# Performance work log

Measured on AMD Instinct MI355X. Metric: run time of the kernel, lower is better.

Reference implementation:

```python
import jax, jax.numpy as jnp
import numpy as np

NUM_EMBEDDINGS = 512
EMBEDDING_DIM = 64
COMMITMENT_COST = 0.25


def setup_inputs() -> dict:
    key = jax.random.key(0)
    k1, k2 = jax.random.split(key)
    inputs = jax.random.normal(k1, (32, 64, 64, 64), dtype=jnp.float32)  # NCHW, C=D
    # torch init: uniform(-1/K, 1/K)
    embeddings = jax.random.uniform(
        k2, (NUM_EMBEDDINGS, EMBEDDING_DIM), dtype=jnp.float32,
        minval=-1.0 / NUM_EMBEDDINGS, maxval=1.0 / NUM_EMBEDDINGS)
    return {"inputs": inputs, "embeddings": embeddings}


def reference(inputs, embeddings):
    # NCHW -> NHWC
    x = jnp.transpose(inputs, (0, 2, 3, 1))
    B, H, W, D = x.shape
    flat = x.reshape(-1, D)  # [N, D]
    # squared L2 distances to codebook: [N, K]
    distances = (jnp.sum(flat * flat, axis=1, keepdims=True)
                 + jnp.sum(embeddings * embeddings, axis=1)
                 - 2.0 * flat @ embeddings.T)
    encoding_indices = jnp.argmin(distances, axis=1)  # [N]
    # one-hot @ codebook in the original == direct gather
    quantized = embeddings[encoding_indices].reshape(B, H, W, D)
    # commitment loss (quantized is detached in original)
    e_latent_loss = jnp.mean((jax.lax.stop_gradient(quantized) - x) ** 2)
    loss = COMMITMENT_COST * e_latent_loss
    # straight-through estimator
    quantized_st = x + jax.lax.stop_gradient(quantized - x)
    out = jnp.transpose(quantized_st, (0, 3, 1, 2))  # back to NCHW
    return out, loss, encoding_indices.reshape(B, H, W)
```

## Files before the change

### kernel.cpp

```cpp
#include <hip/hip_runtime.h>
#include <math.h>

#define NUM_K 512
#define DIM   64
#define HW    4096
#define IMG   (DIM * HW)
#define OUT_Q 8388608
#define LOSS_OFF OUT_Q
#define IDX_OFF (OUT_Q + 1)
#define DELTA 8e-5f

#define WS_EH   0
#define WS_EL   65536
#define WS_SE   131072
#define WS_CNT  133120
#define WS_PART 133376
#define WS_ET   137472
#define WS_WL   268544

typedef float f32x4 __attribute__((ext_vector_type(4)));
typedef short s8v   __attribute__((ext_vector_type(8)));

__device__ inline short f2bf(float f) {
  unsigned u = __float_as_uint(f);
  return (short)((u + 0x7FFF + ((u >> 16) & 1)) >> 16);
}
__device__ inline float bf2f(short s) {
  return __uint_as_float(((unsigned)(unsigned short)s) << 16);
}

__global__ void vq_prep(const float* __restrict__ emb, char* __restrict__ ws) {
  short* eh = (short*)(ws + WS_EH);
  short* el = (short*)(ws + WS_EL);
  float* se = (float*)(ws + WS_SE);
  float* et = (float*)(ws + WS_ET);
  __shared__ float ebuf[64][65];
  const int tid = threadIdx.x;
  const int kb  = blockIdx.x * 64;
  if (blockIdx.x == 0 && tid == 0) *(int*)(ws + WS_CNT) = 0;
#pragma unroll
  for (int i = 0; i < 64; ++i)
    ebuf[i][tid] = emb[(size_t)(kb + i) * DIM + tid];
  __syncthreads();
  const int k = kb + tid;
  float s = 0.f;
#pragma unroll
  for (int j = 0; j < DIM; ++j) {
    const float v = ebuf[tid][j];
    s = fmaf(v, v, s);
    const short h = f2bf(v);
    eh[k * DIM + j] = h;
    el[k * DIM + j] = f2bf(v - bf2f(h));
    et[j * NUM_K + k] = v;
  }
  se[k] = s;
}

__launch_bounds__(512, 4)
__global__ void vq_main(const float* __restrict__ in, const float* __restrict__ emb,
                        char* __restrict__ ws, float* __restrict__ out, int wlcap) {
  const short* eh = (const short*)(ws + WS_EH);
  const short* el = (const short*)(ws + WS_EL);
  const float* se = (const float*)(ws + WS_SE);
  int* wcnt  = (int*)(ws + WS_CNT);
  int* wlist = (int*)(ws + WS_WL);
  double* partial = (double*)(ws + WS_PART);
  __shared__ float m1s[2][256], m2s[2][256];
  __shared__ int   bkbuf[256];
  __shared__ double red[8];

  const int tid  = threadIdx.x;
  const int lane = tid & 63, w = tid >> 6;
  const int side = w >> 2;
  const int wq   = w & 3;
  const int l15 = lane & 15, lh = lane >> 4;
  const int d0 = lh * 8;
  const int pblk = blockIdx.x * 256;
  const int n = pblk >> 12;
  const int hwb = pblk & 4095;
  const int p0 = wq * 64;

  s8v ah[4][2], al[4][2];
#pragma unroll
  for (int rt = 0; rt < 4; ++rt) {
    const float* xp = in + (size_t)n * IMG + hwb + (p0 + rt * 16 + l15);
#pragma unroll
    for (int h = 0; h < 2; ++h) {
      s8v vh, vl;
#pragma unroll
      for (int j = 0; j < 8; ++j) {
        const float xv = xp[(h * 32 + d0 + j) * HW];
        const short hi = f2bf(xv);
        vh[j] = hi;
        vl[j] = f2bf(xv - bf2f(hi));
      }
      ah[rt][h] = vh; al[rt][h] = vl;
    }
  }

  float m1[4][4], m2[4][4];
#pragma unroll
  for (int rt = 0; rt < 4; ++rt)
#pragma unroll
    for (int r = 0; r < 4; ++r) { m1[rt][r] = INFINITY; m2[rt][r] = INFINITY; }

  for (int ct = 0; ct < 16; ++ct) {
    const int c = side * 256 + ct * 16 + l15;
    const s8v beh0 = *(const s8v*)(eh + c * DIM + d0);
    const s8v beh1 = *(const s8v*)(eh + c * DIM + 32 + d0);
    const s8v bel0 = *(const s8v*)(el + c * DIM + d0);
    const s8v bel1 = *(const s8v*)(el + c * DIM + 32 + d0);
    const float sec = se[c];
#pragma unroll
    for (int rt = 0; rt < 4; ++rt) {
      f32x4 acc = {0.f, 0.f, 0.f, 0.f};
      acc = __builtin_amdgcn_mfma_f32_16x16x32_bf16(ah[rt][0], beh0, acc, 0, 0, 0);
      acc = __builtin_amdgcn_mfma_f32_16x16x32_bf16(ah[rt][1], beh1, acc, 0, 0, 0);
      acc = __builtin_amdgcn_mfma_f32_16x16x32_bf16(al[rt][0], beh0, acc, 0, 0, 0);
      acc = __builtin_amdgcn_mfma_f32_16x16x32_bf16(al[rt][1], beh1, acc, 0, 0, 0);
      acc = __builtin_amdgcn_mfma_f32_16x16x32_bf16(ah[rt][0], bel0, acc, 0, 0, 0);
      acc = __builtin_amdgcn_mfma_f32_16x16x32_bf16(ah[rt][1], bel1, acc, 0, 0, 0);
#pragma unroll
      for (int r = 0; r < 4; ++r) {
        const float cv = fmaf(-2.f, acc[r], sec);
        const float pk = __int_as_float((__float_as_int(cv) & 0xFFFFFE00) | c);
        m2[rt][r] = fminf(m2[rt][r], fmaxf(m1[rt][r], pk));
        m1[rt][r] = fminf(m1[rt][r], pk);
      }
    }
  }

#pragma unroll
  for (int s = 1; s < 16; s <<= 1) {
#pragma unroll
    for (int rt = 0; rt < 4; ++rt)
#pragma unroll
      for (int r = 0; r < 4; ++r) {
        const float o1 = __shfl_xor(m1[rt][r], s);
        const float o2 = __shfl_xor(m2[rt][r], s);
        const float hi = fmaxf(m1[rt][r], o1);
        m1[rt][r] = fminf(m1[rt][r], o1);
        m2[rt][r] = fminf(fminf(m2[rt][r], o2), hi);
      }
  }
  if (l15 == 0) {
#pragma unroll
    for (int rt = 0; rt < 4; ++rt)
#pragma unroll
      for (int r = 0; r < 4; ++r) {
        const int lp = p0 + rt * 16 + lh * 4 + r;
        m1s[side][lp] = m1[rt][r];
        m2s[side][lp] = m2[rt][r];
      }
  }
  __syncthreads();

  if (tid < 256) {
    const float m1a = m1s[0][tid], m1b = m1s[1][tid];
    const float m2a = m2s[0][tid], m2b = m2s[1][tid];
    const float mm1 = fminf(m1a, m1b);
    const float mm2 = fminf(fminf(m2a, m2b), fmaxf(m1a, m1b));
    const int bk = __float_as_int(mm1) & 511;
    bkbuf[tid] = bk;
    out[IDX_OFF + pblk + tid] = (float)bk;
    const int flagv = (mm2 - mm1 <= DELTA) ? 1 : 0;
    const unsigned long long b = __ballot(flagv);
    const int cnt = __popcll(b);
    int base = 0;
    if (lane == 0 && cnt) base = atomicAdd(wcnt, cnt);
    base = __shfl(base, 0);
    if (flagv) {
      const int pos = base + __popcll(b & ((1ull << lane) - 1));
      if (pos < wlcap) wlist[pos] = pblk + tid;
    }
  }
  __syncthreads();

  float ls = 0.f;
#pragma unroll
  for (int rt = 0; rt < 4; ++rt) {
    const int lp = p0 + rt * 16 + l15;
    const int bk = bkbuf[lp];
    const float* ep = emb + bk * DIM + side * 32 + d0;
    const f32x4 q0 = *(const f32x4*)ep;
    const f32x4 q1 = *(const f32x4*)(ep + 4);
    float* op = out + (size_t)n * IMG + (size_t)(side * 32 + d0) * HW + hwb + lp;
    const s8v vh = ah[rt][side], vl = al[rt][side];
#pragma unroll
    for (int j = 0; j < 8; ++j) {
      const float q = (j < 4) ? q0[j] : q1[j - 4];
      op[j * HW] = q;
      const float xv = bf2f(vh[j]) + bf2f(vl[j]);
      const float dd = q - xv;
      ls = fmaf(dd, dd, ls);
    }
  }
  double dls = (double)ls;
#pragma unroll
  for (int o = 32; o; o >>= 1) dls += __shfl_down(dls, o);
  if (lane == 0) red[w] = dls;
  __syncthreads();
  if (tid == 0) {
    double t = 0.0;
#pragma unroll
    for (int q = 0; q < 8; ++q) t += red[q];
    partial[blockIdx.x] = t;
  }
}

__launch_bounds__(512)
__global__ void vq_fix(const float* __restrict__ in, const float* __restrict__ emb,
                       char* __restrict__ ws, float* __restrict__ out, int wlcap) {
  const float* se = (const float*)(ws + WS_SE);
  const float* et = (const float*)(ws + WS_ET);
  const int* wlist = (const int*)(ws + WS_WL);
  double* partial = (double*)(ws + WS_PART);
  __shared__ float xs[DIM];
  __shared__ float pd[8];
  __shared__ int   pkk[8];
  __shared__ int   sbk;

  const int tid = threadIdx.x;
  const int lane = tid & 63, w = tid >> 6;
  int M = *(const int*)(ws + WS_CNT);
  if (M > wlcap) M = wlcap;

  for (int i = blockIdx.x; i < M; i += gridDim.x) {
    const int p = wlist[i];
    const int n = p >> 12, hw = p & 4095;
    if (tid < DIM)
      xs[tid] = in[(size_t)n * IMG + (size_t)tid * HW + hw];
    __syncthreads();

    float sx = 0.f, a = 0.f;
#pragma unroll 8
    for (int j = 0; j < DIM; ++j) {
      const float xj = xs[j];
      sx = fmaf(xj, xj, sx);
      a  = fmaf(xj, et[j * NUM_K + tid], a);
    }
    float bd = (sx + se[tid]) - 2.f * a;
    int bki = tid;
#pragma unroll
    for (int s = 1; s < 64; s <<= 1) {
      const float od = __shfl_xor(bd, s);
      const int   oi = __shfl_xor(bki, s);
      const bool t = (od < bd) || (od == bd && oi < bki);
      bd = t ? od : bd; bki = t ? oi : bki;
    }
    if (lane == 0) { pd[w] = bd; pkk[w] = bki; }
    __syncthreads();
    if (tid == 0) {
      float fb = pd[0]; int fk = pkk[0];
#pragma unroll
      for (int q = 1; q < 8; ++q)
        if (pd[q] < fb) { fb = pd[q]; fk = pkk[q]; }
      sbk = fk;
    }
    __syncthreads();
    const int bkn = sbk;
    const int oldk = (int)out[IDX_OFF + p];
    if (bkn != oldk && tid < DIM) {
      const float xj = xs[tid];
      const float qn = emb[bkn  * DIM + tid];
      const float qo = emb[oldk * DIM + tid];
      out[(size_t)n * IMG + (size_t)tid * HW + hw] = qn;
      const float dl = (qn - xj) * (qn - xj) - (qo - xj) * (qo - xj);
      double dd = (double)dl;
#pragma unroll
      for (int o = 32; o; o >>= 1) dd += __shfl_down(dd, o);
      if (tid == 0) {
        atomicAdd(&partial[0], dd);
        out[IDX_OFF + p] = (float)bkn;
      }
    }
    __syncthreads();
  }
}

__global__ void vq_loss(const double* __restrict__ partial, float* __restrict__ out) {
  __shared__ double r2[4];
  const int tid = threadIdx.x;
  double s = partial[tid] + partial[tid + 256];
#pragma unroll
  for (int o = 32; o; o >>= 1) s += __shfl_down(s, o);
  if ((tid & 63) == 0) r2[tid >> 6] = s;
  __syncthreads();
  if (tid == 0) {
    const double t = r2[0] + r2[1] + r2[2] + r2[3];
    out[LOSS_OFF] = (float)(0.25 * t / (double)OUT_Q);
  }
}

extern "C" void kernel_launch(void* const* d_in, const int* in_sizes, int n_in,
                              void* d_out, int out_size, void* d_ws, size_t ws_size,
                              hipStream_t stream) {
  (void)in_sizes; (void)n_in; (void)out_size;
  const float* in  = (const float*)d_in[0];
  const float* emb = (const float*)d_in[1];
  float* out = (float*)d_out;
  char* ws = (char*)d_ws;
  size_t avail = ws_size > WS_WL ? ws_size - WS_WL : 0;
  int wlcap = (int)(avail / 4 < 131072 ? avail / 4 : 131072);
  vq_prep<<<8,    64,  0, stream>>>(emb, ws);
  vq_main<<<512,  512, 0, stream>>>(in, emb, ws, out, wlcap);
  vq_fix <<<2048, 512, 0, stream>>>(in, emb, ws, out, wlcap);
  vq_loss<<<1,    256, 0, stream>>>((const double*)(ws + WS_PART), out);
}
```

Measured before the change: 191.7 us.

## Restructure VQ main kernel: full codebook per wave, smaller blocks, more blocks

Each wave now scans all 512 codes for 32 pixels instead of splitting the codebook across two wave halves. This removes the cross-half shared-memory merge of min/second-min and one barrier stage. Blocks shrink to 256 threads covering 128 pixels, with 1024 blocks launched, and the partial-sum array and workspace offsets grow to match. The fix kernel grid is also cut from 2048 to 512 blocks. Codebook reuse per wave loads drops (2 row tiles instead of 4), which may raise L2 traffic for codebook fragments.

```diff
diff --git a/kernel.cpp b/kernel.cpp
--- a/kernel.cpp
+++ b/kernel.cpp
@@ -9,14 +9,15 @@
 #define LOSS_OFF OUT_Q
 #define IDX_OFF (OUT_Q + 1)
 #define DELTA 8e-5f
+#define NBLK  1024
 
 #define WS_EH   0
 #define WS_EL   65536
 #define WS_SE   131072
 #define WS_CNT  133120
 #define WS_PART 133376
-#define WS_ET   137472
-#define WS_WL   268544
+#define WS_ET   141568
+#define WS_WL   272640
 
 typedef float f32x4 __attribute__((ext_vector_type(4)));
 typedef short s8v   __attribute__((ext_vector_type(8)));
@@ -56,7 +57,7 @@
   se[k] = s;
 }
 
-__launch_bounds__(512, 4)
+__launch_bounds__(256, 4)
 __global__ void vq_main(const float* __restrict__ in, const float* __restrict__ emb,
                         char* __restrict__ ws, float* __restrict__ out, int wlcap) {
   const short* eh = (const short*)(ws + WS_EH);
@@ -65,24 +66,22 @@
   int* wcnt  = (int*)(ws + WS_CNT);
   int* wlist = (int*)(ws + WS_WL);
   double* partial = (double*)(ws + WS_PART);
-  __shared__ float m1s[2][256], m2s[2][256];
-  __shared__ int   bkbuf[256];
-  __shared__ double red[8];
+  __shared__ int bkbuf[128];
+  __shared__ unsigned char flg[128];
+  __shared__ double red[4];
 
   const int tid  = threadIdx.x;
   const int lane = tid & 63, w = tid >> 6;
-  const int side = w >> 2;
-  const int wq   = w & 3;
   const int l15 = lane & 15, lh = lane >> 4;
   const int d0 = lh * 8;
-  const int pblk = blockIdx.x * 256;
+  const int pblk = blockIdx.x * 128;
   const int n = pblk >> 12;
   const int hwb = pblk & 4095;
-  const int p0 = wq * 64;
-
-  s8v ah[4][2], al[4][2];
-#pragma unroll
-  for (int rt = 0; rt < 4; ++rt) {
+  const int p0 = w * 32;
+
+  s8v ah[2][2], al[2][2];
+#pragma unroll
+  for (int rt = 0; rt < 2; ++rt) {
     const float* xp = in + (size_t)n * IMG + hwb + (p0 + rt * 16 + l15);
 #pragma unroll
     for (int h = 0; h < 2; ++h) {
@@ -98,21 +97,21 @@
     }
   }
 
-  float m1[4][4], m2[4][4];
-#pragma unroll
-  for (int rt = 0; rt < 4; ++rt)
+  float m1[2][4], m2[2][4];
+#pragma unroll
+  for (int rt = 0; rt < 2; ++rt)
 #pragma unroll
     for (int r = 0; r < 4; ++r) { m1[rt][r] = INFINITY; m2[rt][r] = INFINITY; }
 
-  for (int ct = 0; ct < 16; ++ct) {
-    const int c = side * 256 + ct * 16 + l15;
+  for (int ct = 0; ct < 32; ++ct) {
+    const int c = ct * 16 + l15;
     const s8v beh0 = *(const s8v*)(eh + c * DIM + d0);
     const s8v beh1 = *(const s8v*)(eh + c * DIM + 32 + d0);
     const s8v bel0 = *(const s8v*)(el + c * DIM + d0);
     const s8v bel1 = *(const s8v*)(el + c * DIM + 32 + d0);
     const float sec = se[c];
 #pragma unroll
-    for (int rt = 0; rt < 4; ++rt) {
+    for (int rt = 0; rt < 2; ++rt) {
       f32x4 acc = {0.f, 0.f, 0.f, 0.f};
       acc = __builtin_amdgcn_mfma_f32_16x16x32_bf16(ah[rt][0], beh0, acc, 0, 0, 0);
       acc = __builtin_amdgcn_mfma_f32_16x16x32_bf16(ah[rt][1], beh1, acc, 0, 0, 0);
@@ -133,7 +132,7 @@
 #pragma unroll
   for (int s = 1; s < 16; s <<= 1) {
 #pragma unroll
-    for (int rt = 0; rt < 4; ++rt)
+    for (int rt = 0; rt < 2; ++rt)
 #pragma unroll
       for (int r = 0; r < 4; ++r) {
         const float o1 = __shfl_xor(m1[rt][r], s);
@@ -145,31 +144,26 @@
   }
   if (l15 == 0) {
 #pragma unroll
-    for (int rt = 0; rt < 4; ++rt)
+    for (int rt = 0; rt < 2; ++rt)
 #pragma unroll
       for (int r = 0; r < 4; ++r) {
         const int lp = p0 + rt * 16 + lh * 4 + r;
-        m1s[side][lp] = m1[rt][r];
-        m2s[side][lp] = m2[rt][r];
-      }
-  }
-  __syncthreads();
-
-  if (tid < 256) {
-    const float m1a = m1s[0][tid], m1b = m1s[1][tid];
-    const float m2a = m2s[0][tid], m2b = m2s[1][tid];
-    const float mm1 = fminf(m1a, m1b);
-    const float mm2 = fminf(fminf(m2a, m2b), fmaxf(m1a, m1b));
-    const int bk = __float_as_int(mm1) & 511;
-    bkbuf[tid] = bk;
+        bkbuf[lp] = __float_as_int(m1[rt][r]) & 511;
+        flg[lp] = (m2[rt][r] - m1[rt][r] <= DELTA) ? 1 : 0;
+      }
+  }
+  __syncthreads();
+
+  if (tid < 128) {
+    const int bk = bkbuf[tid];
     out[IDX_OFF + pblk + tid] = (float)bk;
-    const int flagv = (mm2 - mm1 <= DELTA) ? 1 : 0;
-    const unsigned long long b = __ballot(flagv);
+    const int f = flg[tid];
+    const unsigned long long b = __ballot(f);
     const int cnt = __popcll(b);
     int base = 0;
     if (lane == 0 && cnt) base = atomicAdd(wcnt, cnt);
     base = __shfl(base, 0);
-    if (flagv) {
+    if (f) {
       const int pos = base + __popcll(b & ((1ull << lane) - 1));
       if (pos < wlcap) wlist[pos] = pblk + tid;
     }
@@ -178,21 +172,24 @@
 
   float ls = 0.f;
 #pragma unroll
-  for (int rt = 0; rt < 4; ++rt) {
+  for (int rt = 0; rt < 2; ++rt) {
     const int lp = p0 + rt * 16 + l15;
     const int bk = bkbuf[lp];
-    const float* ep = emb + bk * DIM + side * 32 + d0;
-    const f32x4 q0 = *(const f32x4*)ep;
-    const f32x4 q1 = *(const f32x4*)(ep + 4);
-    float* op = out + (size_t)n * IMG + (size_t)(side * 32 + d0) * HW + hwb + lp;
-    const s8v vh = ah[rt][side], vl = al[rt][side];
-#pragma unroll
-    for (int j = 0; j < 8; ++j) {
-      const float q = (j < 4) ? q0[j] : q1[j - 4];
-      op[j * HW] = q;
-      const float xv = bf2f(vh[j]) + bf2f(vl[j]);
-      const float dd = q - xv;
-      ls = fmaf(dd, dd, ls);
+#pragma unroll
+    for (int h = 0; h < 2; ++h) {
+      const float* ep = emb + bk * DIM + h * 32 + d0;
+      const f32x4 q0 = *(const f32x4*)ep;
+      const f32x4 q1 = *(const f32x4*)(ep + 4);
+      float* op = out + (size_t)n * IMG + (size_t)(h * 32 + d0) * HW + hwb + lp;
+      const s8v vh = ah[rt][h], vl = al[rt][h];
+#pragma unroll
+      for (int j = 0; j < 8; ++j) {
+        const float q = (j < 4) ? q0[j] : q1[j - 4];
+        op[j * HW] = q;
+        const float xv = bf2f(vh[j]) + bf2f(vl[j]);
+        const float dd = q - xv;
+        ls = fmaf(dd, dd, ls);
+      }
     }
   }
   double dls = (double)ls;
@@ -200,12 +197,7 @@
   for (int o = 32; o; o >>= 1) dls += __shfl_down(dls, o);
   if (lane == 0) red[w] = dls;
   __syncthreads();
-  if (tid == 0) {
-    double t = 0.0;
-#pragma unroll
-    for (int q = 0; q < 8; ++q) t += red[q];
-    partial[blockIdx.x] = t;
-  }
+  if (tid == 0) partial[blockIdx.x] = red[0] + red[1] + red[2] + red[3];
 }
 
 __launch_bounds__(512)
@@ -281,7 +273,7 @@
 __global__ void vq_loss(const double* __restrict__ partial, float* __restrict__ out) {
   __shared__ double r2[4];
   const int tid = threadIdx.x;
-  double s = partial[tid] + partial[tid + 256];
+  double s = partial[tid] + partial[tid + 256] + partial[tid + 512] + partial[tid + 768];
 #pragma unroll
   for (int o = 32; o; o >>= 1) s += __shfl_down(s, o);
   if ((tid & 63) == 0) r2[tid >> 6] = s;
@@ -303,7 +295,7 @@
   size_t avail = ws_size > WS_WL ? ws_size - WS_WL : 0;
   int wlcap = (int)(avail / 4 < 131072 ? avail / 4 : 131072);
   vq_prep<<<8,    64,  0, stream>>>(emb, ws);
-  vq_main<<<512,  512, 0, stream>>>(in, emb, ws, out, wlcap);
-  vq_fix <<<2048, 512, 0, stream>>>(in, emb, ws, out, wlcap);
+  vq_main<<<NBLK, 256, 0, stream>>>(in, emb, ws, out, wlcap);
+  vq_fix <<<512,  512, 0, stream>>>(in, emb, ws, out, wlcap);
   vq_loss<<<1,    256, 0, stream>>>((const double*)(ws + WS_PART), out);
 }
```

Measured after the change: 182.7 us. -4.7%, faster.
